# Kernel tuning notes

Hardware: AMD Instinct MI355X
Metric: run time of the kernel (lower is better)

The kernel has to match this reference:

```python
import jax, jax.numpy as jnp
import numpy as np

B, L, D, N = 8, 1024, 1024, 32  # N = d_state // 2 (complex conjugate-pair modes)
DT_MIN, DT_MAX = 0.001, 0.1


def setup_inputs() -> dict:
    key = jax.random.key(0)
    ks = jax.random.split(key, 12)
    s = 1.0 / np.sqrt(D)  # torch Linear / Conv1d default init bound
    inp = {
        "x": jax.random.normal(ks[0], (B, L, D), jnp.float32),
        "in_W": jax.random.uniform(ks[1], (D, D), jnp.float32, -s, s),
        "in_b": jax.random.uniform(ks[2], (D,), jnp.float32, -s, s),
        # S4D kernel params
        "log_dt": (np.log(DT_MIN)
                   + jax.random.uniform(ks[3], (D,), jnp.float32)
                   * (np.log(DT_MAX) - np.log(DT_MIN))).astype(jnp.float32),
        "C": jax.random.normal(ks[4], (D, N, 2), jnp.float32),  # complex C as (re, im)
        "log_A_real": jnp.log(0.5 * jnp.ones((D, N), jnp.float32)),
        "A_imag": jnp.tile((np.pi * jnp.arange(N, dtype=np.float32))[None, :], (D, 1)),
        "D_skip": jax.random.normal(ks[5], (D,), jnp.float32),
        # output_linear = Conv1d(D, 2D, 1) + GLU(dim=-2); kernel squeezed to (2D, D)
        "glu_W": jax.random.uniform(ks[6], (2 * D, D), jnp.float32, -s, s),
        "glu_b": jax.random.uniform(ks[7], (2 * D,), jnp.float32, -s, s),
        "out_W": jax.random.uniform(ks[8], (D, D), jnp.float32, -s, s),
        "out_b": jax.random.uniform(ks[9], (D,), jnp.float32, -s, s),
    }
    return inp


def reference(x, in_W, in_b, log_dt, C, log_A_real, A_imag, D_skip,
              glu_W, glu_b, out_W, out_b):
    # in_proj
    x_in = x @ in_W.T + in_b                      # (B, L, D)
    u = jnp.swapaxes(x_in, 1, 2)                  # (B, D, L) -- transposed=False path
    Lseq = u.shape[-1]

    # ---- S4D kernel (ZOH-like discretization of diagonal SSM) ----
    dt = jnp.exp(log_dt)                          # (D,)
    Cc = (C[..., 0] + 1j * C[..., 1]).astype(jnp.complex64)   # (D, N)
    A = (-jnp.exp(log_A_real) + 1j * A_imag).astype(jnp.complex64)
    dtA = A * dt[:, None].astype(jnp.complex64)   # (D, N)
    # Vandermonde: exp(dtA * l) for l in [0, L)
    K = jnp.exp(dtA[:, :, None] * jnp.arange(Lseq, dtype=jnp.float32))  # (D, N, L)
    Ceff = Cc * (jnp.exp(dtA) - 1.0) / A
    k = 2.0 * jnp.einsum('hn,hnl->hl', Ceff, K).real            # (D, L)

    # ---- FFT causal convolution ----
    n = 2 * Lseq
    k_f = jnp.fft.rfft(k, n=n)                    # (D, L+1)
    u_f = jnp.fft.rfft(u, n=n)                    # (B, D, L+1)
    y = jnp.fft.irfft(u_f * k_f, n=n)[..., :Lseq] # (B, D, L)

    y = y + u * D_skip[:, None]                   # skip connection
    y = jax.nn.gelu(y, approximate=False)         # torch nn.GELU (erf)

    # Conv1d(D, 2D, kernel=1) + GLU over channel dim
    z = jnp.einsum('oh,bhl->bol', glu_W, y) + glu_b[None, :, None]
    a, g = jnp.split(z, 2, axis=1)
    y = a * jax.nn.sigmoid(g)                     # (B, D, L)

    y = jnp.swapaxes(y, 1, 2)                     # (B, L, D)
    out = y @ out_W.T + out_b
    return out + x
```

## Files before the change

### kernel.cpp

```cpp
#include <hip/hip_runtime.h>
#include <math.h>

#define BB 8
#define LL 1024
#define DD 1024
#define KD 1024
#define NM 32
#define NCH 16
#define CL 64
#define NTOK (BB * LL)

typedef __bf16 bf16_t;
typedef __bf16 bf16x8 __attribute__((ext_vector_type(8)));
typedef __bf16 bf16x4 __attribute__((ext_vector_type(4)));
typedef float  f32x4  __attribute__((ext_vector_type(4)));

__device__ __forceinline__ float gelu_f(float z)
{
    float t = fmaf(0.044715f * z * z, z, z);
    return z / (1.f + expf(-1.5957691216f * t));
}

__global__ __launch_bounds__(256)
void f2b_all_kernel(const float* __restrict__ x,    bf16_t* __restrict__ xb,
                    const float* __restrict__ w0,   bf16_t* __restrict__ d0,
                    const float* __restrict__ w1,   bf16_t* __restrict__ d1,
                    const float* __restrict__ w2,   bf16_t* __restrict__ d2)
{
    int b = blockIdx.x;
    const float* s; bf16_t* d; int base;
    if (b < 8192)       { s = x;  d = xb; base = b; }
    else if (b < 9216)  { s = w0; d = d0; base = b - 8192; }
    else if (b < 11264) { s = w1; d = d1; base = b - 9216; }
    else                { s = w2; d = d2; base = b - 11264; }
    int i = (base * 256 + threadIdx.x) * 4;
    float4 f = *(const float4*)(s + i);
    bf16x4 o = { (bf16_t)f.x, (bf16_t)f.y, (bf16_t)f.z, (bf16_t)f.w };
    *(bf16x4*)(d + i) = o;
}

__device__ __forceinline__ void stage128x32(const bf16_t* __restrict__ g,
                                            bf16_t* lds, int tid)
{
    #pragma unroll
    for (int q = 0; q < 2; ++q) {
        const bf16_t* src = g + (size_t)(q * 64 + (tid >> 2)) * KD + (tid & 3) * 8;
        bf16_t* dst = lds + q * 2048 + tid * 8;
        __builtin_amdgcn_global_load_lds(
            (const __attribute__((address_space(1))) void*)src,
            (__attribute__((address_space(3))) void*)dst, 16, 0, 0);
    }
}

template<int MODE>
__global__ __launch_bounds__(256)
void gemm_bk64_kernel(const bf16_t* __restrict__ A, const bf16_t* __restrict__ B,
                      const float* __restrict__ bias, const float* __restrict__ res,
                      void* __restrict__ outp, int ldo)
{
    __shared__ bf16_t As[2][128 * 32];
    __shared__ bf16_t Bs[2][128 * 32];
    const int tid = threadIdx.x;
    const int lane = tid & 63, w = tid >> 6;
    const int wy = w >> 1, wx = w & 1;
    const int m0 = blockIdx.y << 7, n0 = blockIdx.x << 7;
    const bf16_t* Ag = A + (size_t)m0 * KD;
    const bf16_t* Bg = B + (size_t)n0 * KD;
    f32x4 acc[4][4] = {};
    const int lm = lane & 15;
    const int ks = (lane >> 4) << 3;

    for (int k0 = 0; k0 < KD; k0 += 64) {
        stage128x32(Ag + k0,      As[0], tid);
        stage128x32(Bg + k0,      Bs[0], tid);
        stage128x32(Ag + k0 + 32, As[1], tid);
        stage128x32(Bg + k0 + 32, Bs[1], tid);
        __syncthreads();
        #pragma unroll
        for (int p = 0; p < 2; ++p) {
            bf16x8 af[4], bfr[4];
            #pragma unroll
            for (int i = 0; i < 4; ++i)
                af[i] = *(bf16x8*)&As[p][((wy << 6) + (i << 4) + lm) * 32 + ks];
            #pragma unroll
            for (int j = 0; j < 4; ++j)
                bfr[j] = *(bf16x8*)&Bs[p][((wx << 6) + (j << 4) + lm) * 32 + ks];
            #pragma unroll
            for (int i = 0; i < 4; ++i)
                #pragma unroll
                for (int j = 0; j < 4; ++j)
                    acc[i][j] = __builtin_amdgcn_mfma_f32_16x16x32_bf16(
                                    af[i], bfr[j], acc[i][j], 0, 0, 0);
        }
        __syncthreads();
    }

    const int row4 = (lane >> 4) << 2;
    #pragma unroll
    for (int i = 0; i < 4; ++i) {
        #pragma unroll
        for (int r = 0; r < 4; ++r) {
            int m = m0 + (wy << 6) + (i << 4) + row4 + r;
            #pragma unroll
            for (int j = 0; j < 4; ++j) {
                int n = n0 + (wx << 6) + (j << 4) + lm;
                float v = acc[i][j][r];
                if (MODE == 0) {
                    ((bf16_t*)outp)[(size_t)m * ldo + n] = (bf16_t)(v + bias[m]);
                } else if (MODE == 1) {
                    ((bf16_t*)outp)[(size_t)m * ldo + n] = (bf16_t)(v + bias[n]);
                } else {
                    ((float*)outp)[(size_t)m * ldo + n] =
                        v + bias[n] + res[(size_t)m * ldo + n];
                }
            }
        }
    }
}

__global__ __launch_bounds__(256)
void glu_combine_kernel(const bf16_t* __restrict__ z, bf16_t* __restrict__ v)
{
    int i = blockIdx.x * 256 + threadIdx.x;
    int m = i >> 7, n8 = (i & 127) << 3;
    const bf16_t* zp = z + (size_t)m * 2048 + n8;
    bf16x8 za = *(const bf16x8*)zp;
    bf16x8 zg = *(const bf16x8*)(zp + 1024);
    bf16x8 o;
    #pragma unroll
    for (int e = 0; e < 8; ++e) {
        float a = (float)za[e], gg = (float)zg[e];
        o[e] = (bf16_t)(a / (1.f + expf(-gg)));
    }
    *(bf16x8*)(v + (size_t)m * 1024 + n8) = o;
}

__global__ __launch_bounds__(64)
void genV_kernel(const float* __restrict__ log_dt, const float* __restrict__ lar,
                 const float* __restrict__ aim, bf16_t* __restrict__ V)
{
    const int tid = threadIdx.x;
    const int h = blockIdx.x * 2 + (tid >> 5);
    const int n = tid & 31;
    const float dt = expf(log_dt[h]);
    const float ardt = -expf(lar[h * NM + n]) * dt;
    const float aidt = aim[h * NM + n] * dt;
    float sn, cs;
    sincosf(aidt, &sn, &cs);
    float er = expf(ardt);
    float wr = er * cs, wi = er * sn;
    float inv = 1.f / fmaf(wr, wr, wi * wi);
    float vr = wr * inv, vi = -wi * inv;
    sincosf(63.f * aidt, &sn, &cs);
    er = expf(63.f * ardt);
    float pr = er * cs, pi = er * sn;
    bf16_t* rowr = V + ((size_t)h * 64 + 2 * n) * 64;
    bf16_t* rowi = rowr + 64;
    #pragma unroll
    for (int c8 = 0; c8 < 8; ++c8) {
        bf16x8 rr, ri;
        #pragma unroll
        for (int e = 0; e < 8; ++e) {
            rr[e] = (bf16_t)pr; ri[e] = (bf16_t)pi;
            float t = fmaf(pr, vr, -pi * vi);
            pi = fmaf(pr, vi, pi * vr);
            pr = t;
        }
        *(bf16x8*)(rowr + c8 * 8) = rr;
        *(bf16x8*)(rowi + c8 * 8) = ri;
    }
}

__global__ __launch_bounds__(64)
void genTP_kernel(const float* __restrict__ log_dt, const float* __restrict__ lar,
                  const float* __restrict__ aim, const float* __restrict__ Cp,
                  const float* __restrict__ dskip, bf16_t* __restrict__ TP)
{
    __shared__ float ardt_s[NM], aidt_s[NM], cr_s[NM], ci_s[NM], K_s[CL];
    const int h = blockIdx.x;
    const int tid = threadIdx.x;
    const float dt = expf(log_dt[h]);
    if (tid < NM) {
        int n = tid;
        float ar = -expf(lar[h * NM + n]);
        float ai = aim[h * NM + n];
        float sn, cs;
        sincosf(ai * dt, &sn, &cs);
        float er = expf(ar * dt);
        float wrr = er * cs, wii = er * sn;
        float Crr = Cp[(h * NM + n) * 2 + 0];
        float Cii = Cp[(h * NM + n) * 2 + 1];
        float nr = fmaf(Crr, wrr - 1.f, -Cii * wii);
        float ni = fmaf(Crr, wii, Cii * (wrr - 1.f));
        float inv = 2.f / fmaf(ar, ar, ai * ai);
        cr_s[n] = fmaf(nr, ar, ni * ai) * inv;
        ci_s[n] = fmaf(ni, ar, -nr * ai) * inv;
        ardt_s[n] = ar * dt;
        aidt_s[n] = ai * dt;
    }
    __syncthreads();
    {
        float d = (float)tid;
        float kv = (tid == 0) ? dskip[h] : 0.f;
        #pragma unroll 8
        for (int n = 0; n < NM; ++n) {
            float sn, cs;
            sincosf(aidt_s[n] * d, &sn, &cs);
            float e = expf(ardt_s[n] * d);
            kv = fmaf(cr_s[n], e * cs, kv);
            kv = fmaf(-ci_s[n], e * sn, kv);
        }
        K_s[tid] = kv;
    }
    __syncthreads();
    const int i = tid;
    bf16_t* row = TP + ((size_t)h * CL + i) * 128;
    #pragma unroll
    for (int c8 = 0; c8 < 8; ++c8) {
        bf16x8 v;
        #pragma unroll
        for (int e = 0; e < 8; ++e) {
            int l = c8 * 8 + e;
            v[e] = (l <= i) ? (bf16_t)K_s[i - l] : (bf16_t)0.f;
        }
        *(bf16x8*)(row + c8 * 8) = v;
    }
    const float fi = (float)(i + 1);
    #pragma unroll
    for (int c8 = 0; c8 < 8; ++c8) {
        bf16x8 v;
        #pragma unroll
        for (int q = 0; q < 4; ++q) {
            int n = c8 * 4 + q;
            float sn, cs;
            sincosf(aidt_s[n] * fi, &sn, &cs);
            float e = expf(ardt_s[n] * fi);
            float Wr = e * cs, Wi = e * sn;
            v[2 * q]     = (bf16_t)(fmaf(cr_s[n], Wr, -ci_s[n] * Wi));
            v[2 * q + 1] = (bf16_t)(-fmaf(cr_s[n], Wi, ci_s[n] * Wr));
        }
        *(bf16x8*)(row + 64 + c8 * 8) = v;
    }
}

__global__ __launch_bounds__(256)
void g1_kernel(const bf16_t* __restrict__ u_ch, const bf16_t* __restrict__ V,
               float* __restrict__ Sbc)
{
    const int h = blockIdx.x;
    const int tid = threadIdx.x;
    const int lane = tid & 63, w = tid >> 6;
    const int lm = lane & 15, ks = (lane >> 4) << 3;
    const bf16_t* U  = u_ch + (size_t)h * 8192;
    const bf16_t* Vh = V    + (size_t)h * 4096;
    f32x4 acc[2][4] = {};
    #pragma unroll
    for (int kk = 0; kk < 2; ++kk) {
        int k0 = kk * 32;
        bf16x8 af[2], bfr[4];
        #pragma unroll
        for (int im = 0; im < 2; ++im)
            af[im] = *(const bf16x8*)(U + (((w << 1) + im) * 16 + lm) * 64 + k0 + ks);
        #pragma unroll
        for (int jn = 0; jn < 4; ++jn)
            bfr[jn] = *(const bf16x8*)(Vh + (jn * 16 + lm) * 64 + k0 + ks);
        #pragma unroll
        for (int im = 0; im < 2; ++im)
            #pragma unroll
            for (int jn = 0; jn < 4; ++jn)
                acc[im][jn] = __builtin_amdgcn_mfma_f32_16x16x32_bf16(
                                  af[im], bfr[jn], acc[im][jn], 0, 0, 0);
    }
    float* out = Sbc + (size_t)h * 8192;
    const int r4 = (lane >> 4) << 2;
    #pragma unroll
    for (int im = 0; im < 2; ++im)
        #pragma unroll
        for (int jn = 0; jn < 4; ++jn)
            #pragma unroll
            for (int r = 0; r < 4; ++r) {
                int batch = ((w << 1) + im) * 16 + r4 + r;
                int comp  = jn * 16 + lm;
                out[batch * 64 + comp] = acc[im][jn][r];
            }
}

__global__ __launch_bounds__(256)
void passB_kernel(const float* __restrict__ Sbc, const float* __restrict__ log_dt,
                  const float* __restrict__ lar, const float* __restrict__ aim,
                  bf16_t* __restrict__ Sc)
{
    const int tid = threadIdx.x;
    const int gid = blockIdx.x * 8 + (tid >> 5);
    const int h = gid >> 3, b = gid & 7;
    const int n = tid & 31;
    const float dt = expf(log_dt[h]);
    const float ardt = -expf(lar[h * NM + n]) * dt;
    const float aidt = aim[h * NM + n] * dt;
    float sn, cs;
    sincosf(64.f * aidt, &sn, &cs);
    float er = expf(64.f * ardt);
    const float gr = er * cs, gi = er * sn;
    float sr = 0.f, si = 0.f;
    for (int c = 0; c < NCH; ++c) {
        size_t base = (size_t)h * 8192 + (b * 16 + c) * 64 + 2 * n;
        float2 lv = *(const float2*)(Sbc + base);
        Sc[base]     = (bf16_t)sr;
        Sc[base + 1] = (bf16_t)si;
        float t = fmaf(gr, sr, fmaf(-gi, si, lv.x));
        si = fmaf(gr, si, fmaf(gi, sr, lv.y));
        sr = t;
    }
}

__global__ __launch_bounds__(256)
void g3_kernel(const bf16_t* __restrict__ u_ch, const bf16_t* __restrict__ Sc,
               const bf16_t* __restrict__ TP, bf16_t* __restrict__ y_bi)
{
    const int h = blockIdx.x;
    const int tid = threadIdx.x;
    const int lane = tid & 63, w = tid >> 6;
    const int lm = lane & 15, ks = (lane >> 4) << 3;
    const bf16_t* U   = u_ch + (size_t)h * 8192;
    const bf16_t* Sch = Sc   + (size_t)h * 8192;
    const bf16_t* TPh = TP   + (size_t)h * 8192;
    f32x4 acc[2][4] = {};
    #pragma unroll
    for (int kk = 0; kk < 4; ++kk) {
        const bf16_t* Ab = (kk < 2) ? (U + kk * 32) : (Sch + (kk - 2) * 32);
        bf16x8 af[2], bfr[4];
        #pragma unroll
        for (int im = 0; im < 2; ++im)
            af[im] = *(const bf16x8*)(Ab + (((w << 1) + im) * 16 + lm) * 64 + ks);
        #pragma unroll
        for (int jn = 0; jn < 4; ++jn)
            bfr[jn] = *(const bf16x8*)(TPh + (jn * 16 + lm) * 128 + kk * 32 + ks);
        #pragma unroll
        for (int im = 0; im < 2; ++im)
            #pragma unroll
            for (int jn = 0; jn < 4; ++jn)
                acc[im][jn] = __builtin_amdgcn_mfma_f32_16x16x32_bf16(
                                  af[im], bfr[jn], acc[im][jn], 0, 0, 0);
    }
    bf16_t* out = y_bi + (size_t)h * 8192;
    const int r4 = (lane >> 4) << 2;
    #pragma unroll
    for (int im = 0; im < 2; ++im)
        #pragma unroll
        for (int jn = 0; jn < 4; ++jn)
            #pragma unroll
            for (int r = 0; r < 4; ++r) {
                int batch = ((w << 1) + im) * 16 + r4 + r;
                int i = jn * 16 + lm;
                out[batch * 64 + i] = (bf16_t)gelu_f(acc[im][jn][r]);
            }
}

__global__ __launch_bounds__(256)
void transpose_kernel(const bf16_t* __restrict__ src, bf16_t* __restrict__ dst,
                      int src_rows, int src_cols)
{
    __shared__ unsigned short tile[64][68];
    const int tid = threadIdx.x;
    const int c0 = blockIdx.x << 6, r0 = blockIdx.y << 6;
    const int r = tid >> 4, c4 = (tid & 15) << 2;
    #pragma unroll
    for (int p = 0; p < 4; ++p) {
        int rr = p * 16 + r;
        ushort4 v = *(const ushort4*)((const unsigned short*)src +
                                      (size_t)(r0 + rr) * src_cols + c0 + c4);
        *(ushort4*)&tile[rr][c4] = v;
    }
    __syncthreads();
    #pragma unroll
    for (int p = 0; p < 4; ++p) {
        int rr = p * 16 + r;
        ushort4 v;
        v.x = tile[c4 + 0][rr];
        v.y = tile[c4 + 1][rr];
        v.z = tile[c4 + 2][rr];
        v.w = tile[c4 + 3][rr];
        *(ushort4*)((unsigned short*)dst + (size_t)(c0 + rr) * src_rows + r0 + c4) = v;
    }
}

extern "C" void kernel_launch(void* const* d_in, const int* in_sizes, int n_in,
                              void* d_out, int out_size, void* d_ws, size_t ws_size,
                              hipStream_t stream)
{
    (void)in_sizes; (void)n_in; (void)out_size; (void)ws_size;
    const float* x      = (const float*)d_in[0];
    const float* in_W   = (const float*)d_in[1];
    const float* in_b   = (const float*)d_in[2];
    const float* log_dt = (const float*)d_in[3];
    const float* Cp     = (const float*)d_in[4];
    const float* lar    = (const float*)d_in[5];
    const float* aim    = (const float*)d_in[6];
    const float* dsk    = (const float*)d_in[7];
    const float* gluW   = (const float*)d_in[8];
    const float* glub   = (const float*)d_in[9];
    const float* outW   = (const float*)d_in[10];
    const float* outb   = (const float*)d_in[11];

    char* ws = (char*)d_ws;
    bf16_t* xb    = (bf16_t*)(ws);
    bf16_t* TP    = (bf16_t*)(ws);
    bf16_t* y_tok = (bf16_t*)(ws);
    bf16_t* vb    = (bf16_t*)(ws);
    bf16_t* V     = (bf16_t*)(ws + 16777216);
    bf16_t* Sc    = (bf16_t*)(ws + 16777216);
    bf16_t* z     = (bf16_t*)(ws + 16777216);
    bf16_t* u_ch  = (bf16_t*)(ws + 33554432);
    bf16_t* wbin  = (bf16_t*)(ws + 50331648);
    bf16_t* wbglu = (bf16_t*)(ws + 52428800);
    bf16_t* wbout = (bf16_t*)(ws + 56623104);
    float*  Sbc   = (float*)d_out;
    bf16_t* y_bi  = (bf16_t*)d_out;

    f2b_all_kernel<<<dim3(12288), dim3(256), 0, stream>>>(
        x, xb, in_W, wbin, gluW, wbglu, outW, wbout);

    gemm_bk64_kernel<0><<<dim3(NTOK / 128, DD / 128), dim3(256), 0, stream>>>(
        wbin, xb, in_b, nullptr, u_ch, NTOK);

    genV_kernel <<<dim3(DD / 2), dim3(64), 0, stream>>>(log_dt, lar, aim, V);
    genTP_kernel<<<dim3(DD),     dim3(64), 0, stream>>>(log_dt, lar, aim, Cp, dsk, TP);
    g1_kernel   <<<dim3(DD), dim3(256), 0, stream>>>(u_ch, V, Sbc);
    passB_kernel<<<dim3(DD * BB / 8), dim3(256), 0, stream>>>(Sbc, log_dt, lar, aim, Sc);
    g3_kernel   <<<dim3(DD), dim3(256), 0, stream>>>(u_ch, Sc, TP, y_bi);

    transpose_kernel<<<dim3(NTOK / 64, DD / 64), dim3(256), 0, stream>>>(y_bi, y_tok, DD, NTOK);
    gemm_bk64_kernel<1><<<dim3(2048 / 128, NTOK / 128), dim3(256), 0, stream>>>(
        y_tok, wbglu, glub, nullptr, z, 2048);
    glu_combine_kernel<<<dim3(NTOK * DD / 8 / 256), dim3(256), 0, stream>>>(z, vb);
    gemm_bk64_kernel<2><<<dim3(DD / 128, NTOK / 128), dim3(256), 0, stream>>>(
        vb, wbout, outb, x, d_out, DD);
}
```

Baseline: 309.6 us.

## Fuse SSM chunk GEMM, state scan and output GEMM into one kernel

Merges g1, passB and g3 into a single per-channel kernel that keeps chunk-end states and scanned states in shared memory, and reuses the u fragments already held in registers across both MFMA stages. It also merges genV and genTP into one launch that branches on block index. This removes the global round-trips for Sbc and Sc and cuts the launch count by three. The cost is 48 KB of shared memory per block, which may limit occupancy, plus a serial scan phase between two barriers.

```diff
diff --git a/kernel.cpp b/kernel.cpp
--- a/kernel.cpp
+++ b/kernel.cpp
@@ -136,49 +136,46 @@
 }
 
 __global__ __launch_bounds__(64)
-void genV_kernel(const float* __restrict__ log_dt, const float* __restrict__ lar,
-                 const float* __restrict__ aim, bf16_t* __restrict__ V)
+void genVTP_kernel(const float* __restrict__ log_dt, const float* __restrict__ lar,
+                   const float* __restrict__ aim, const float* __restrict__ Cp,
+                   const float* __restrict__ dskip,
+                   bf16_t* __restrict__ V, bf16_t* __restrict__ TP)
 {
     const int tid = threadIdx.x;
-    const int h = blockIdx.x * 2 + (tid >> 5);
-    const int n = tid & 31;
-    const float dt = expf(log_dt[h]);
-    const float ardt = -expf(lar[h * NM + n]) * dt;
-    const float aidt = aim[h * NM + n] * dt;
-    float sn, cs;
-    sincosf(aidt, &sn, &cs);
-    float er = expf(ardt);
-    float wr = er * cs, wi = er * sn;
-    float inv = 1.f / fmaf(wr, wr, wi * wi);
-    float vr = wr * inv, vi = -wi * inv;
-    sincosf(63.f * aidt, &sn, &cs);
-    er = expf(63.f * ardt);
-    float pr = er * cs, pi = er * sn;
-    bf16_t* rowr = V + ((size_t)h * 64 + 2 * n) * 64;
-    bf16_t* rowi = rowr + 64;
-    #pragma unroll
-    for (int c8 = 0; c8 < 8; ++c8) {
-        bf16x8 rr, ri;
-        #pragma unroll
-        for (int e = 0; e < 8; ++e) {
-            rr[e] = (bf16_t)pr; ri[e] = (bf16_t)pi;
-            float t = fmaf(pr, vr, -pi * vi);
-            pi = fmaf(pr, vi, pi * vr);
-            pr = t;
-        }
-        *(bf16x8*)(rowr + c8 * 8) = rr;
-        *(bf16x8*)(rowi + c8 * 8) = ri;
-    }
-}
-
-__global__ __launch_bounds__(64)
-void genTP_kernel(const float* __restrict__ log_dt, const float* __restrict__ lar,
-                  const float* __restrict__ aim, const float* __restrict__ Cp,
-                  const float* __restrict__ dskip, bf16_t* __restrict__ TP)
-{
+    if (blockIdx.x < DD / 2) {
+        const int h = blockIdx.x * 2 + (tid >> 5);
+        const int n = tid & 31;
+        const float dt = expf(log_dt[h]);
+        const float ardt = -expf(lar[h * NM + n]) * dt;
+        const float aidt = aim[h * NM + n] * dt;
+        float sn, cs;
+        sincosf(aidt, &sn, &cs);
+        float er = expf(ardt);
+        float wr = er * cs, wi = er * sn;
+        float inv = 1.f / fmaf(wr, wr, wi * wi);
+        float vr = wr * inv, vi = -wi * inv;
+        sincosf(63.f * aidt, &sn, &cs);
+        er = expf(63.f * ardt);
+        float pr = er * cs, pi = er * sn;
+        bf16_t* rowr = V + ((size_t)h * 64 + 2 * n) * 64;
+        bf16_t* rowi = rowr + 64;
+        #pragma unroll
+        for (int c8 = 0; c8 < 8; ++c8) {
+            bf16x8 rr, ri;
+            #pragma unroll
+            for (int e = 0; e < 8; ++e) {
+                rr[e] = (bf16_t)pr; ri[e] = (bf16_t)pi;
+                float t = fmaf(pr, vr, -pi * vi);
+                pi = fmaf(pr, vi, pi * vr);
+                pr = t;
+            }
+            *(bf16x8*)(rowr + c8 * 8) = rr;
+            *(bf16x8*)(rowi + c8 * 8) = ri;
+        }
+        return;
+    }
     __shared__ float ardt_s[NM], aidt_s[NM], cr_s[NM], ci_s[NM], K_s[CL];
-    const int h = blockIdx.x;
-    const int tid = threadIdx.x;
+    const int h = blockIdx.x - DD / 2;
     const float dt = expf(log_dt[h]);
     if (tid < NM) {
         int n = tid;
@@ -244,94 +241,88 @@
 }
 
 __global__ __launch_bounds__(256)
-void g1_kernel(const bf16_t* __restrict__ u_ch, const bf16_t* __restrict__ V,
-               float* __restrict__ Sbc)
-{
-    const int h = blockIdx.x;
-    const int tid = threadIdx.x;
-    const int lane = tid & 63, w = tid >> 6;
-    const int lm = lane & 15, ks = (lane >> 4) << 3;
-    const bf16_t* U  = u_ch + (size_t)h * 8192;
-    const bf16_t* Vh = V    + (size_t)h * 4096;
-    f32x4 acc[2][4] = {};
-    #pragma unroll
-    for (int kk = 0; kk < 2; ++kk) {
-        int k0 = kk * 32;
-        bf16x8 af[2], bfr[4];
-        #pragma unroll
-        for (int im = 0; im < 2; ++im)
-            af[im] = *(const bf16x8*)(U + (((w << 1) + im) * 16 + lm) * 64 + k0 + ks);
-        #pragma unroll
-        for (int jn = 0; jn < 4; ++jn)
-            bfr[jn] = *(const bf16x8*)(Vh + (jn * 16 + lm) * 64 + k0 + ks);
-        #pragma unroll
-        for (int im = 0; im < 2; ++im)
-            #pragma unroll
-            for (int jn = 0; jn < 4; ++jn)
-                acc[im][jn] = __builtin_amdgcn_mfma_f32_16x16x32_bf16(
-                                  af[im], bfr[jn], acc[im][jn], 0, 0, 0);
-    }
-    float* out = Sbc + (size_t)h * 8192;
-    const int r4 = (lane >> 4) << 2;
-    #pragma unroll
-    for (int im = 0; im < 2; ++im)
-        #pragma unroll
-        for (int jn = 0; jn < 4; ++jn)
-            #pragma unroll
-            for (int r = 0; r < 4; ++r) {
-                int batch = ((w << 1) + im) * 16 + r4 + r;
-                int comp  = jn * 16 + lm;
-                out[batch * 64 + comp] = acc[im][jn][r];
-            }
-}
-
-__global__ __launch_bounds__(256)
-void passB_kernel(const float* __restrict__ Sbc, const float* __restrict__ log_dt,
-                  const float* __restrict__ lar, const float* __restrict__ aim,
-                  bf16_t* __restrict__ Sc)
-{
-    const int tid = threadIdx.x;
-    const int gid = blockIdx.x * 8 + (tid >> 5);
-    const int h = gid >> 3, b = gid & 7;
-    const int n = tid & 31;
-    const float dt = expf(log_dt[h]);
-    const float ardt = -expf(lar[h * NM + n]) * dt;
-    const float aidt = aim[h * NM + n] * dt;
-    float sn, cs;
-    sincosf(64.f * aidt, &sn, &cs);
-    float er = expf(64.f * ardt);
-    const float gr = er * cs, gi = er * sn;
-    float sr = 0.f, si = 0.f;
-    for (int c = 0; c < NCH; ++c) {
-        size_t base = (size_t)h * 8192 + (b * 16 + c) * 64 + 2 * n;
-        float2 lv = *(const float2*)(Sbc + base);
-        Sc[base]     = (bf16_t)sr;
-        Sc[base + 1] = (bf16_t)si;
-        float t = fmaf(gr, sr, fmaf(-gi, si, lv.x));
-        si = fmaf(gr, si, fmaf(gi, sr, lv.y));
-        sr = t;
-    }
-}
-
-__global__ __launch_bounds__(256)
-void g3_kernel(const bf16_t* __restrict__ u_ch, const bf16_t* __restrict__ Sc,
-               const bf16_t* __restrict__ TP, bf16_t* __restrict__ y_bi)
-{
+void ssm_fused_kernel(const bf16_t* __restrict__ u_ch, const bf16_t* __restrict__ V,
+                      const bf16_t* __restrict__ TP,
+                      const float* __restrict__ log_dt, const float* __restrict__ lar,
+                      const float* __restrict__ aim, bf16_t* __restrict__ y_bi)
+{
+    __shared__ float  Sbc_s[128 * 64];
+    __shared__ bf16_t Sc_s[128 * 64];
     const int h = blockIdx.x;
     const int tid = threadIdx.x;
     const int lane = tid & 63, w = tid >> 6;
     const int lm = lane & 15, ks = (lane >> 4) << 3;
     const bf16_t* U   = u_ch + (size_t)h * 8192;
-    const bf16_t* Sch = Sc   + (size_t)h * 8192;
+    const bf16_t* Vh  = V    + (size_t)h * 4096;
     const bf16_t* TPh = TP   + (size_t)h * 8192;
-    f32x4 acc[2][4] = {};
+
+    bf16x8 af_u[2][2];
+    #pragma unroll
+    for (int im = 0; im < 2; ++im)
+        #pragma unroll
+        for (int kk = 0; kk < 2; ++kk)
+            af_u[im][kk] = *(const bf16x8*)(U + (((w << 1) + im) * 16 + lm) * 64
+                                            + kk * 32 + ks);
+
+    f32x4 acc1[2][4] = {};
+    #pragma unroll
+    for (int kk = 0; kk < 2; ++kk) {
+        bf16x8 bfr[4];
+        #pragma unroll
+        for (int jn = 0; jn < 4; ++jn)
+            bfr[jn] = *(const bf16x8*)(Vh + (jn * 16 + lm) * 64 + kk * 32 + ks);
+        #pragma unroll
+        for (int im = 0; im < 2; ++im)
+            #pragma unroll
+            for (int jn = 0; jn < 4; ++jn)
+                acc1[im][jn] = __builtin_amdgcn_mfma_f32_16x16x32_bf16(
+                                   af_u[im][kk], bfr[jn], acc1[im][jn], 0, 0, 0);
+    }
+    const int r4 = (lane >> 4) << 2;
+    #pragma unroll
+    for (int im = 0; im < 2; ++im)
+        #pragma unroll
+        for (int jn = 0; jn < 4; ++jn)
+            #pragma unroll
+            for (int r = 0; r < 4; ++r)
+                Sbc_s[(((w << 1) + im) * 16 + r4 + r) * 64 + jn * 16 + lm]
+                    = acc1[im][jn][r];
+    __syncthreads();
+
+    {
+        const int b = tid >> 5, n = tid & 31;
+        const float dtv = expf(log_dt[h]);
+        const float ardt = -expf(lar[h * NM + n]) * dtv;
+        const float aidt = aim[h * NM + n] * dtv;
+        float sn, cs;
+        sincosf(64.f * aidt, &sn, &cs);
+        float er = expf(64.f * ardt);
+        const float gr = er * cs, gi = er * sn;
+        float sr = 0.f, si = 0.f;
+        for (int c = 0; c < NCH; ++c) {
+            int idx = (b * 16 + c) * 64 + 2 * n;
+            float lr = Sbc_s[idx], li = Sbc_s[idx + 1];
+            Sc_s[idx]     = (bf16_t)sr;
+            Sc_s[idx + 1] = (bf16_t)si;
+            float t0 = fmaf(gr, sr, fmaf(-gi, si, lr));
+            si = fmaf(gr, si, fmaf(gi, sr, li));
+            sr = t0;
+        }
+    }
+    __syncthreads();
+
+    f32x4 acc2[2][4] = {};
     #pragma unroll
     for (int kk = 0; kk < 4; ++kk) {
-        const bf16_t* Ab = (kk < 2) ? (U + kk * 32) : (Sch + (kk - 2) * 32);
         bf16x8 af[2], bfr[4];
         #pragma unroll
-        for (int im = 0; im < 2; ++im)
-            af[im] = *(const bf16x8*)(Ab + (((w << 1) + im) * 16 + lm) * 64 + ks);
+        for (int im = 0; im < 2; ++im) {
+            if (kk < 2)
+                af[im] = af_u[im][kk];
+            else
+                af[im] = *(bf16x8*)&Sc_s[(((w << 1) + im) * 16 + lm) * 64
+                                         + (kk - 2) * 32 + ks];
+        }
         #pragma unroll
         for (int jn = 0; jn < 4; ++jn)
             bfr[jn] = *(const bf16x8*)(TPh + (jn * 16 + lm) * 128 + kk * 32 + ks);
@@ -339,11 +330,10 @@
         for (int im = 0; im < 2; ++im)
             #pragma unroll
             for (int jn = 0; jn < 4; ++jn)
-                acc[im][jn] = __builtin_amdgcn_mfma_f32_16x16x32_bf16(
-                                  af[im], bfr[jn], acc[im][jn], 0, 0, 0);
+                acc2[im][jn] = __builtin_amdgcn_mfma_f32_16x16x32_bf16(
+                                   af[im], bfr[jn], acc2[im][jn], 0, 0, 0);
     }
     bf16_t* out = y_bi + (size_t)h * 8192;
-    const int r4 = (lane >> 4) << 2;
     #pragma unroll
     for (int im = 0; im < 2; ++im)
         #pragma unroll
@@ -352,7 +342,7 @@
             for (int r = 0; r < 4; ++r) {
                 int batch = ((w << 1) + im) * 16 + r4 + r;
                 int i = jn * 16 + lm;
-                out[batch * 64 + i] = (bf16_t)gelu_f(acc[im][jn][r]);
+                out[batch * 64 + i] = (bf16_t)gelu_f(acc2[im][jn][r]);
             }
 }
 
@@ -408,13 +398,11 @@
     bf16_t* y_tok = (bf16_t*)(ws);
     bf16_t* vb    = (bf16_t*)(ws);
     bf16_t* V     = (bf16_t*)(ws + 16777216);
-    bf16_t* Sc    = (bf16_t*)(ws + 16777216);
     bf16_t* z     = (bf16_t*)(ws + 16777216);
     bf16_t* u_ch  = (bf16_t*)(ws + 33554432);
     bf16_t* wbin  = (bf16_t*)(ws + 50331648);
     bf16_t* wbglu = (bf16_t*)(ws + 52428800);
     bf16_t* wbout = (bf16_t*)(ws + 56623104);
-    float*  Sbc   = (float*)d_out;
     bf16_t* y_bi  = (bf16_t*)d_out;
 
     f2b_all_kernel<<<dim3(12288), dim3(256), 0, stream>>>(
@@ -423,11 +411,10 @@
     gemm_bk64_kernel<0><<<dim3(NTOK / 128, DD / 128), dim3(256), 0, stream>>>(
         wbin, xb, in_b, nullptr, u_ch, NTOK);
 
-    genV_kernel <<<dim3(DD / 2), dim3(64), 0, stream>>>(log_dt, lar, aim, V);
-    genTP_kernel<<<dim3(DD),     dim3(64), 0, stream>>>(log_dt, lar, aim, Cp, dsk, TP);
-    g1_kernel   <<<dim3(DD), dim3(256), 0, stream>>>(u_ch, V, Sbc);
-    passB_kernel<<<dim3(DD * BB / 8), dim3(256), 0, stream>>>(Sbc, log_dt, lar, aim, Sc);
-    g3_kernel   <<<dim3(DD), dim3(256), 0, stream>>>(u_ch, Sc, TP, y_bi);
+    genVTP_kernel<<<dim3(DD / 2 + DD), dim3(64), 0, stream>>>(
+        log_dt, lar, aim, Cp, dsk, V, TP);
+    ssm_fused_kernel<<<dim3(DD), dim3(256), 0, stream>>>(
+        u_ch, V, TP, log_dt, lar, aim, y_bi);
 
     transpose_kernel<<<dim3(NTOK / 64, DD / 64), dim3(256), 0, stream>>>(y_bi, y_tok, DD, NTOK);
     gemm_bk64_kernel<1><<<dim3(2048 / 128, NTOK / 128), dim3(256), 0, stream>>>(
```

New measurement: 286.2 us. 1.08x faster.
